# Kernel tuning notes

Hardware: AMD Instinct MI355X
Metric: run time of the kernel (lower is better)

The kernel has to match this reference:

```python
import jax, jax.numpy as jnp
from jax import lax
import numpy as np

B, S, D_CTX = 32, 384, 300
H = 600            # hard-coded in the torch module (torch.zeros([1, 600]))
IN = D_CTX + 3     # context + 3-dim BIO tag embedding


def setup_inputs() -> dict:
    key = jax.random.key(0)
    ks = jax.random.split(key, 12)
    sc = lambda *sh: 1.0 / np.sqrt(sh[-1])
    return {
        "context": jax.random.normal(ks[0], (B, S, D_CTX), jnp.float32),
        "answer_tags": jax.random.randint(ks[1], (B, 1, S), 0, 3),
        "bio_emb": jax.random.normal(ks[2], (3, 3), jnp.float32),
        # GRUCell params (torch layout: W_ih [3H, IN], W_hh [3H, H])
        "W_ih": jax.random.normal(ks[3], (3 * H, IN), jnp.float32) * sc(3 * H, IN),
        "b_ih": jax.random.normal(ks[4], (3 * H,), jnp.float32) * 0.01,
        "W_hh": jax.random.normal(ks[5], (3 * H, H), jnp.float32) * sc(3 * H, H),
        "b_hh": jax.random.normal(ks[6], (3 * H,), jnp.float32) * 0.01,
        "W_lin": jax.random.normal(ks[7], (2 * H, 2 * H), jnp.float32) * sc(2 * H, 2 * H),
        "b_lin": jnp.zeros((2 * H,), jnp.float32),
        "W_g": jax.random.normal(ks[8], (2 * H, 4 * H), jnp.float32) * sc(2 * H, 4 * H),
        "b_g": jnp.zeros((2 * H,), jnp.float32),
        "W_f": jax.random.normal(ks[9], (2 * H, 4 * H), jnp.float32) * sc(2 * H, 4 * H),
        "b_f": jnp.zeros((2 * H,), jnp.float32),
    }


def _gru_scan(xs, W_ih, b_ih, W_hh, b_hh):
    # xs: [T, IN]; hidden carries across ALL steps (the torch code never resets
    # the hidden state between batch elements -- faithful quirk).
    gi_all = xs @ W_ih.T + b_ih            # [T, 3H] precomputed input projections

    def step(h, gi):
        gh = h @ W_hh.T + b_hh             # [3H]
        ir, iz, inn = jnp.split(gi, 3)
        hr, hz, hn = jnp.split(gh, 3)
        r = jax.nn.sigmoid(ir + hr)
        z = jax.nn.sigmoid(iz + hz)
        n = jnp.tanh(inn + r * hn)
        h_new = (1.0 - z) * n + z * h
        return h_new, h_new

    h0 = jnp.zeros((H,), xs.dtype)
    h_last, hs = lax.scan(step, h0, gi_all)
    return h_last, hs                      # [H], [T, H]


def reference(context, answer_tags, bio_emb, W_ih, b_ih, W_hh, b_hh,
              W_lin, b_lin, W_g, b_g, W_f, b_f):
    b, s, _ = context.shape
    tags = bio_emb[answer_tags[:, 0, :]]                    # [B, S, 3]
    emb = jnp.concatenate([tags, context], axis=-1)          # [B, S, IN]

    # Forward direction: one continuous scan over all B*S steps (hidden not reset).
    h_f, fwd = _gru_scan(emb.reshape(b * s, -1), W_ih, b_ih, W_hh, b_hh)
    forward_states = fwd.reshape(b, s, H)

    # Backward direction: words reversed within each batch element; the torch
    # code stores backward_states[b, w] = state after processing word S-1-w.
    h_b, bwd = _gru_scan(emb[:, ::-1, :].reshape(b * s, -1), W_ih, b_ih, W_hh, b_hh)
    backward_states = bwd.reshape(b, s, H)

    all_h = jnp.concatenate([forward_states, backward_states], axis=-1)  # [B,S,2H]

    # calc_attention: the inner state_idx loop OVERWRITES attn[b,:,:] each
    # iteration, so only the LAST state (index S-1) survives, broadcast over S.
    hs = all_h[:, -1, :]                                     # [B, 2H]
    q = hs @ W_lin.T + b_lin                                 # [B, 2H]
    scores = jax.nn.softmax(jnp.einsum('bd,bsd->bs', q, all_h), axis=-1)
    ctx = jnp.einsum('bs,bsd->bd', scores, all_h)            # [B, 2H]
    cat = jnp.concatenate([ctx, hs], axis=-1)                # [B, 4H]
    g = jax.nn.sigmoid(cat @ W_g.T + b_g)
    f = jnp.tanh(cat @ W_f.T + b_f)
    gated = g * f + (1.0 - g) * hs                           # [B, 2H]
    attn = jnp.broadcast_to(gated[:, None, :], (b, s, 2 * H))

    final = jnp.concatenate([h_f, h_b])[None, :]             # [1, 2H]
    return final, attn
```

## Files before the change

kernel.cpp:

```cpp
#include <hip/hip_runtime.h>
#include <math.h>

#define TT    12288
#define HH    600
#define GG    1800
#define INP   303
#define INP_P 304
#define BB    32
#define SS    384
#define D2    1200
#define D4    2400

#define NWG  75
#define JPW  8
#define WROW 608

#define SENT   0xAAAAAAAAu
#define SENT64 0xAAAAAAAAAAAAAAAAull

#define EMB_OFF    0ull
#define WP_OFF     3735552ull
#define GI_OFF     4282752ull
#define HS_OFF     26403808ull
#define Q_OFF      26442208ull
#define CTX_OFF    26480608ull
#define GATED_OFF  26519008ull
#define P_OFF      0ull

__global__ void build_emb(const float* __restrict__ ctx, const int* __restrict__ tags,
                          const float* __restrict__ bio, float* __restrict__ emb) {
    int idx = blockIdx.x * 256 + threadIdx.x;
    if (idx >= TT * INP_P) return;
    int row = idx / INP_P;
    int c = idx - row * INP_P;
    float v;
    if (c < 3)        v = bio[tags[row] * 3 + c];
    else if (c < INP) v = ctx[(size_t)row * 300 + (c - 3)];
    else              v = 0.f;
    emb[idx] = v;
}

__global__ void pad_wih(const float* __restrict__ W, float* __restrict__ Wp) {
    int idx = blockIdx.x * 256 + threadIdx.x;
    if (idx >= GG * INP_P) return;
    int r = idx / INP_P, c = idx - r * INP_P;
    Wp[idx] = (c < INP) ? W[(size_t)r * INP + c] : 0.f;
}

__global__ __launch_bounds__(256) void gemm_gi(const float* __restrict__ A,
                                               const float* __restrict__ Bw,
                                               const float* __restrict__ bias,
                                               float* __restrict__ C) {
    __shared__ float As[16][68];
    __shared__ float Bs[16][68];
    const int tid = threadIdx.x;
    const int bm = blockIdx.x, bn = blockIdx.y;
    const int tx = tid & 15, ty = tid >> 4;
    const int lm = tid >> 2;
    const int lk = (tid & 3) * 4;
    const int gbase = bn * 64;
    float acc[4][4] = {};
    for (int k0 = 0; k0 < INP_P; k0 += 16) {
        float4 av = *(const float4*)(A + (size_t)(bm * 64 + lm) * INP_P + k0 + lk);
        int grow = gbase + lm;
        float4 bv = make_float4(0.f, 0.f, 0.f, 0.f);
        if (grow < GG) bv = *(const float4*)(Bw + (size_t)grow * INP_P + k0 + lk);
        As[lk + 0][lm] = av.x; As[lk + 1][lm] = av.y; As[lk + 2][lm] = av.z; As[lk + 3][lm] = av.w;
        Bs[lk + 0][lm] = bv.x; Bs[lk + 1][lm] = bv.y; Bs[lk + 2][lm] = bv.z; Bs[lk + 3][lm] = bv.w;
        __syncthreads();
#pragma unroll
        for (int kk = 0; kk < 16; ++kk) {
            float4 a4 = *(const float4*)&As[kk][tx * 4];
            float4 b4 = *(const float4*)&Bs[kk][ty * 4];
            acc[0][0] += a4.x * b4.x; acc[0][1] += a4.x * b4.y; acc[0][2] += a4.x * b4.z; acc[0][3] += a4.x * b4.w;
            acc[1][0] += a4.y * b4.x; acc[1][1] += a4.y * b4.y; acc[1][2] += a4.y * b4.z; acc[1][3] += a4.y * b4.w;
            acc[2][0] += a4.z * b4.x; acc[2][1] += a4.z * b4.y; acc[2][2] += a4.z * b4.z; acc[2][3] += a4.z * b4.w;
            acc[3][0] += a4.w * b4.x; acc[3][1] += a4.w * b4.y; acc[3][2] += a4.w * b4.z; acc[3][3] += a4.w * b4.w;
        }
        __syncthreads();
    }
    int g0 = gbase + ty * 4;
    if (g0 < GG) {
        float4 bi4 = *(const float4*)(bias + g0);
#pragma unroll
        for (int i = 0; i < 4; ++i) {
            float4 v = make_float4(acc[i][0] + bi4.x, acc[i][1] + bi4.y,
                                   acc[i][2] + bi4.z, acc[i][3] + bi4.w);
            *(float4*)(C + (size_t)(bm * 64 + tx * 4 + i) * GG + g0) = v;
        }
    }
}

__global__ __launch_bounds__(256) void gru_scan(const float* __restrict__ gi,
                                                const float* __restrict__ Whh,
                                                const float* __restrict__ bhh,
                                                float* __restrict__ out) {
    __shared__ __align__(16) float w_lds[JPW * 3 * WROW];
    __shared__ __align__(16) float h_lds[2][WROW];

    const int tid = threadIdx.x;
    const int chain = blockIdx.x / NWG;
    const int wg = blockIdx.x % NWG;
    const int j0 = wg * JPW;
    const int wave = tid >> 6;
    const int lane = tid & 63;
    const int half = lane >> 5;
    const int s = lane & 31;
    const int j = wave * 2 + half;
    const int jg = j0 + j;

    float* statesOut = out + 1200 + (size_t)chain * TT * 600;
    unsigned long long* statesU64 = (unsigned long long*)statesOut;

    for (int q = tid; q < JPW * 3 * 150; q += 256) {
        int row = q / 150, c4 = (q - row * 150) * 4;
        int jj = row / 3, g = row - jj * 3;
        *(float4*)&w_lds[row * WROW + c4] =
            *(const float4*)(Whh + (size_t)(g * 600 + j0 + jj) * 600 + c4);
    }
    float b_r = 0.f, b_z = 0.f, b_n = 0.f;
    if (s == 0) { b_r = bhh[jg]; b_z = bhh[600 + jg]; b_n = bhh[1200 + jg]; }
    for (int i = tid; i < 2 * WROW; i += 256) h_lds[0][i] = 0.f;
    __syncthreads();

    float gr_c = 0.f, gz_c = 0.f, gn_c = 0.f;
    int si = 0, bi = 0;
    if (s == 0) {
        int r0 = (chain == 0) ? 0 : (SS - 1);
        const float* gp = gi + (size_t)r0 * GG + jg;
        gr_c = gp[0]; gz_c = gp[600]; gn_c = gp[1200];
    }

    float h_own = 0.f;

    for (int t = 0; t < TT; ++t) {
        const int slot = t & 1;
        if (t > 0) {
            if (tid < 150) {
                const unsigned long long* hu = statesU64 + (size_t)(t - 1) * 300 + tid * 2;
                unsigned long long u0, u1;
                for (;;) {
                    u0 = __hip_atomic_load(hu + 0, __ATOMIC_RELAXED, __HIP_MEMORY_SCOPE_AGENT);
                    u1 = __hip_atomic_load(hu + 1, __ATOMIC_RELAXED, __HIP_MEMORY_SCOPE_AGENT);
                    if (u0 != SENT64 && u1 != SENT64) break;
                    __builtin_amdgcn_s_sleep(1);
                }
                float4 hv;
                ((unsigned long long*)&hv)[0] = u0;
                ((unsigned long long*)&hv)[1] = u1;
                *(float4*)&h_lds[slot][tid * 4] = hv;
            }
            __syncthreads();
        }
        float gr_n = gr_c, gz_n = gz_c, gn_n = gn_c;
        int si2 = si + 1, bi2 = bi;
        if (si2 == SS) { si2 = 0; ++bi2; }
        if (s == 0 && t + 1 < TT) {
            int rn = (chain == 0) ? (t + 1) : (bi2 * SS + (SS - 1) - si2);
            const float* gp = gi + (size_t)rn * GG + jg;
            gr_n = gp[0]; gz_n = gp[600]; gn_n = gp[1200];
        }
        float a0 = 0.f, a1 = 0.f, a2 = 0.f;
        if (s < 30) {
            const float* w0 = &w_lds[(j * 3 + 0) * WROW + s * 20];
            const float* w1 = &w_lds[(j * 3 + 1) * WROW + s * 20];
            const float* w2 = &w_lds[(j * 3 + 2) * WROW + s * 20];
            const float* hp = &h_lds[slot][s * 20];
#pragma unroll
            for (int u = 0; u < 5; ++u) {
                float4 hv = *(const float4*)(hp + u * 4);
                float4 x0 = *(const float4*)(w0 + u * 4);
                float4 x1 = *(const float4*)(w1 + u * 4);
                float4 x2 = *(const float4*)(w2 + u * 4);
                a0 += x0.x * hv.x + x0.y * hv.y + x0.z * hv.z + x0.w * hv.w;
                a1 += x1.x * hv.x + x1.y * hv.y + x1.z * hv.z + x1.w * hv.w;
                a2 += x2.x * hv.x + x2.y * hv.y + x2.z * hv.z + x2.w * hv.w;
            }
        }
#pragma unroll
        for (int off = 16; off > 0; off >>= 1) {
            a0 += __shfl_down(a0, off, 32);
            a1 += __shfl_down(a1, off, 32);
            a2 += __shfl_down(a2, off, 32);
        }
        if (s == 0) {
            float r = 1.f / (1.f + __expf(-(gr_c + a0 + b_r)));
            float z = 1.f / (1.f + __expf(-(gz_c + a1 + b_z)));
            float x = gn_c + r * (a2 + b_n);
            float e = __expf(-2.f * fabsf(x));
            float n = copysignf((1.f - e) / (1.f + e), x);
            float hnew = (1.f - z) * n + z * h_own;
            h_own = hnew;
            float partner = __shfl(hnew, (lane + 32) & 63);
            if (half == 0) {
                unsigned long long pk = ((unsigned long long)__float_as_uint(hnew)) |
                                        (((unsigned long long)__float_as_uint(partner)) << 32);
                if (pk == SENT64) pk ^= 1ull;
                __hip_atomic_store(statesU64 + (size_t)t * 300 + (j0 >> 1) + wave, pk,
                                   __ATOMIC_RELAXED, __HIP_MEMORY_SCOPE_AGENT);
            }
            if (t == TT - 1) out[chain * 600 + jg] = hnew;
        }
        gr_c = gr_n; gz_c = gz_n; gn_c = gn_n;
        si = si2; bi = bi2;
    }
}

__global__ __launch_bounds__(256) void attn_qs(const float* __restrict__ Wlin,
                                               const float* __restrict__ blin,
                                               const float* __restrict__ outp,
                                               float* __restrict__ ws) {
    __shared__ float hs_lds[1200];
    const int bi = blockIdx.x, ob = blockIdx.y * 60, tid = threadIdx.x;
    const float* fwdS = outp + 1200;
    const float* bwdS = outp + 1200 + (size_t)TT * 600;
    size_t row = (size_t)(bi * SS + SS - 1) * 600;
    for (int k = tid; k < 600; k += 256) {
        hs_lds[k] = fwdS[row + k];
        hs_lds[600 + k] = bwdS[row + k];
    }
    __syncthreads();
    if (blockIdx.y == 0) {
        float* ws_hs = ws + HS_OFF;
        for (int k = tid; k < 1200; k += 256) ws_hs[bi * 1200 + k] = hs_lds[k];
    }
    float* ws_q = ws + Q_OFF;
    const int wave = tid >> 6, lane = tid & 63;
    for (int i = 0; i < 15; ++i) {
        int o = ob + wave * 15 + i;
        const float* wr = Wlin + (size_t)o * 1200;
        float acc = 0.f;
        for (int k = lane; k < 1200; k += 64) acc += hs_lds[k] * wr[k];
        for (int off = 32; off > 0; off >>= 1) acc += __shfl_down(acc, off);
        if (lane == 0) ws_q[bi * 1200 + o] = acc + blin[o];
    }
}

__global__ __launch_bounds__(256) void attn_logits(const float* __restrict__ outp,
                                                   float* __restrict__ ws) {
    __shared__ float q_lds[1200];
    __shared__ float p_lds[SS];
    __shared__ float red[8];
    const int bi = blockIdx.x, tid = threadIdx.x;
    const float* fwdS = outp + 1200;
    const float* bwdS = outp + 1200 + (size_t)TT * 600;
    const float* ws_q = ws + Q_OFF;
    for (int k = tid; k < 1200; k += 256) q_lds[k] = ws_q[bi * 1200 + k];
    __syncthreads();
    const int wave = tid >> 6, lane = tid & 63;
    for (int s = wave; s < SS; s += 4) {
        size_t base = (size_t)(bi * SS + s) * 600;
        float acc = 0.f;
        for (int k = lane; k < 600; k += 64)
            acc += q_lds[k] * fwdS[base + k] + q_lds[600 + k] * bwdS[base + k];
        for (int off = 32; off > 0; off >>= 1) acc += __shfl_down(acc, off);
        if (lane == 0) p_lds[s] = acc;
    }
    __syncthreads();
    float m = -1e30f;
    for (int i = tid; i < SS; i += 256) m = fmaxf(m, p_lds[i]);
    for (int off = 32; off > 0; off >>= 1) m = fmaxf(m, __shfl_down(m, off));
    if (lane == 0) red[wave] = m;
    __syncthreads();
    m = fmaxf(fmaxf(red[0], red[1]), fmaxf(red[2], red[3]));
    float ssum = 0.f;
    for (int i = tid; i < SS; i += 256) ssum += expf(p_lds[i] - m);
    for (int off = 32; off > 0; off >>= 1) ssum += __shfl_down(ssum, off);
    __syncthreads();
    if (lane == 0) red[wave] = ssum;
    __syncthreads();
    ssum = red[0] + red[1] + red[2] + red[3];
    float inv = 1.f / ssum;
    float* ws_p = ws + P_OFF;
    for (int i = tid; i < SS; i += 256) ws_p[bi * SS + i] = expf(p_lds[i] - m) * inv;
}

__global__ __launch_bounds__(256) void attn_ctxv(const float* __restrict__ outp,
                                                 float* __restrict__ ws) {
    __shared__ float p_lds[SS];
    const int bi = blockIdx.x, d0 = blockIdx.y * 240, tid = threadIdx.x;
    const float* ws_p = ws + P_OFF;
    for (int k = tid; k < SS; k += 256) p_lds[k] = ws_p[bi * SS + k];
    __syncthreads();
    if (tid >= 240) return;
    const int d = d0 + tid;
    const float* fwdS = outp + 1200;
    const float* bwdS = outp + 1200 + (size_t)TT * 600;
    const float* Sb = (d < 600) ? (fwdS + d) : (bwdS + d - 600);
    size_t rbase = (size_t)bi * SS * 600;
    float a0 = 0.f, a1 = 0.f, a2 = 0.f, a3 = 0.f;
#pragma unroll 4
    for (int s = 0; s < SS; s += 4) {
        a0 += p_lds[s + 0] * Sb[rbase + (size_t)(s + 0) * 600];
        a1 += p_lds[s + 1] * Sb[rbase + (size_t)(s + 1) * 600];
        a2 += p_lds[s + 2] * Sb[rbase + (size_t)(s + 2) * 600];
        a3 += p_lds[s + 3] * Sb[rbase + (size_t)(s + 3) * 600];
    }
    (ws + CTX_OFF)[bi * 1200 + d] = (a0 + a1) + (a2 + a3);
}

__global__ __launch_bounds__(256) void attn_gate(const float* __restrict__ Wg,
                                                 const float* __restrict__ bg,
                                                 const float* __restrict__ Wf,
                                                 const float* __restrict__ bf,
                                                 float* __restrict__ ws) {
    __shared__ float cat_lds[2400];
    const int bi = blockIdx.x, ob = blockIdx.y * 60, tid = threadIdx.x;
    const float* ws_ctx = ws + CTX_OFF;
    const float* ws_hs = ws + HS_OFF;
    for (int k = tid; k < 1200; k += 256) {
        cat_lds[k] = ws_ctx[bi * 1200 + k];
        cat_lds[1200 + k] = ws_hs[bi * 1200 + k];
    }
    __syncthreads();
    float* ws_g = ws + GATED_OFF;
    const int wave = tid >> 6, lane = tid & 63;
    for (int i = 0; i < 15; ++i) {
        int o = ob + wave * 15 + i;
        const float* wg = Wg + (size_t)o * D4;
        const float* wf = Wf + (size_t)o * D4;
        float ag = 0.f, af = 0.f;
        for (int k = lane; k < D4; k += 64) {
            float c = cat_lds[k];
            ag += c * wg[k];
            af += c * wf[k];
        }
        for (int off = 32; off > 0; off >>= 1) {
            ag += __shfl_down(ag, off);
            af += __shfl_down(af, off);
        }
        if (lane == 0) {
            float g = 1.f / (1.f + expf(-(ag + bg[o])));
            float f = tanhf(af + bf[o]);
            ws_g[bi * 1200 + o] = g * f + (1.f - g) * cat_lds[1200 + o];
        }
    }
}

__global__ void bcast_attn(const float* __restrict__ ws, float* __restrict__ outp) {
    int idx = blockIdx.x * 256 + threadIdx.x;
    const float4* g4 = (const float4*)(ws + GATED_OFF);
    float4* o4 = (float4*)outp;
    int row = idx / 300;
    int d4 = idx - row * 300;
    int bi = row / SS;
    o4[300 + idx] = g4[bi * 300 + d4];
}

extern "C" void kernel_launch(void* const* d_in, const int* in_sizes, int n_in,
                              void* d_out, int out_size, void* d_ws, size_t ws_size,
                              hipStream_t stream) {
    const float* ctx   = (const float*)d_in[0];
    const int*   tags  = (const int*)d_in[1];
    const float* bio   = (const float*)d_in[2];
    const float* W_ih  = (const float*)d_in[3];
    const float* b_ih  = (const float*)d_in[4];
    const float* W_hh  = (const float*)d_in[5];
    const float* b_hh  = (const float*)d_in[6];
    const float* W_lin = (const float*)d_in[7];
    const float* b_lin = (const float*)d_in[8];
    const float* W_g   = (const float*)d_in[9];
    const float* b_g   = (const float*)d_in[10];
    const float* W_f   = (const float*)d_in[11];
    const float* b_f   = (const float*)d_in[12];
    float* out = (float*)d_out;
    float* ws  = (float*)d_ws;

    hipMemsetAsync(out + 1200, 0xAA, (size_t)2 * TT * 600 * sizeof(float), stream);

    build_emb<<<(TT * INP_P + 255) / 256, 256, 0, stream>>>(ctx, tags, bio, ws + EMB_OFF);
    pad_wih<<<(GG * INP_P + 255) / 256, 256, 0, stream>>>(W_ih, ws + WP_OFF);
    gemm_gi<<<dim3(TT / 64, 29), 256, 0, stream>>>(ws + EMB_OFF, ws + WP_OFF, b_ih, ws + GI_OFF);
    gru_scan<<<2 * NWG, 256, 0, stream>>>(ws + GI_OFF, W_hh, b_hh, out);
    attn_qs<<<dim3(BB, 20), 256, 0, stream>>>(W_lin, b_lin, out, ws);
    attn_logits<<<BB, 256, 0, stream>>>(out, ws);
    attn_ctxv<<<dim3(BB, 5), 256, 0, stream>>>(out, ws);
    attn_gate<<<dim3(BB, 20), 256, 0, stream>>>(W_g, b_g, W_f, b_f, ws);
    bcast_attn<<<14400, 256, 0, stream>>>(ws, out);
}
```

Measured before the change: 22.69 ms.

## Replace per-thread sentinel polling with sharded arrival counters in GRU scan

Each workgroup now bumps one of eight sharded global counters per step, and wave 0 polls those counters until all 75 workgroups of its chain have finished the previous step. It then signals the other waves through an LDS flag. The per-element sentinel loads become a single confirming read with no sleep. The aim is to cut the many scattered global polls on the serial 12288-step recurrence, at the cost of an extra atomic add per step and a counter memset.

New measurement: 26.54 ms. +17.0%, slower.

```diff
diff --git a/kernel.cpp b/kernel.cpp
--- a/kernel.cpp
+++ b/kernel.cpp
@@ -25,6 +25,7 @@
 #define Q_OFF      26442208ull
 #define CTX_OFF    26480608ull
 #define GATED_OFF  26519008ull
+#define COUNT_OFF  26557408ull
 #define P_OFF      0ull
 
 __global__ void build_emb(const float* __restrict__ ctx, const int* __restrict__ tags,
@@ -94,9 +95,11 @@
 __global__ __launch_bounds__(256) void gru_scan(const float* __restrict__ gi,
                                                 const float* __restrict__ Whh,
                                                 const float* __restrict__ bhh,
+                                                float* __restrict__ ws,
                                                 float* __restrict__ out) {
     __shared__ __align__(16) float w_lds[JPW * 3 * WROW];
     __shared__ __align__(16) float h_lds[2][WROW];
+    __shared__ unsigned go_lds;
 
     const int tid = threadIdx.x;
     const int chain = blockIdx.x / NWG;
@@ -111,6 +114,8 @@
 
     float* statesOut = out + 1200 + (size_t)chain * TT * 600;
     unsigned long long* statesU64 = (unsigned long long*)statesOut;
+    unsigned* cnt = (unsigned*)(ws + COUNT_OFF) + (size_t)chain * 512;
+    const unsigned cntk = (lane < 3) ? 10u : 9u;
 
     for (int q = tid; q < JPW * 3 * 150; q += 256) {
         int row = q / 150, c4 = (q - row * 150) * 4;
@@ -121,6 +126,7 @@
     float b_r = 0.f, b_z = 0.f, b_n = 0.f;
     if (s == 0) { b_r = bhh[jg]; b_z = bhh[600 + jg]; b_n = bhh[1200 + jg]; }
     for (int i = tid; i < 2 * WROW; i += 256) h_lds[0][i] = 0.f;
+    if (tid == 0) go_lds = 0u;
     __syncthreads();
 
     float gr_c = 0.f, gz_c = 0.f, gn_c = 0.f;
@@ -136,14 +142,30 @@
     for (int t = 0; t < TT; ++t) {
         const int slot = t & 1;
         if (t > 0) {
+            if (wave == 0) {
+                const unsigned tgt = (unsigned)t * cntk;
+                for (;;) {
+                    bool ok = true;
+                    if (lane < 8)
+                        ok = __hip_atomic_load(cnt + lane * 64, __ATOMIC_RELAXED,
+                                               __HIP_MEMORY_SCOPE_AGENT) >= tgt;
+                    if (__ballot(ok) == ~0ull) break;
+                    __builtin_amdgcn_s_sleep(1);
+                }
+                if (lane == 0)
+                    __hip_atomic_store(&go_lds, (unsigned)t, __ATOMIC_RELAXED,
+                                       __HIP_MEMORY_SCOPE_WORKGROUP);
+            } else if (wave <= 2) {
+                while (__hip_atomic_load(&go_lds, __ATOMIC_RELAXED,
+                                         __HIP_MEMORY_SCOPE_WORKGROUP) < (unsigned)t) {}
+            }
             if (tid < 150) {
                 const unsigned long long* hu = statesU64 + (size_t)(t - 1) * 300 + tid * 2;
-                unsigned long long u0, u1;
-                for (;;) {
+                unsigned long long u0 = __hip_atomic_load(hu + 0, __ATOMIC_RELAXED, __HIP_MEMORY_SCOPE_AGENT);
+                unsigned long long u1 = __hip_atomic_load(hu + 1, __ATOMIC_RELAXED, __HIP_MEMORY_SCOPE_AGENT);
+                while (u0 == SENT64 || u1 == SENT64) {
                     u0 = __hip_atomic_load(hu + 0, __ATOMIC_RELAXED, __HIP_MEMORY_SCOPE_AGENT);
                     u1 = __hip_atomic_load(hu + 1, __ATOMIC_RELAXED, __HIP_MEMORY_SCOPE_AGENT);
-                    if (u0 != SENT64 && u1 != SENT64) break;
-                    __builtin_amdgcn_s_sleep(1);
                 }
                 float4 hv;
                 ((unsigned long long*)&hv)[0] = u0;
@@ -201,6 +223,9 @@
             }
             if (t == TT - 1) out[chain * 600 + jg] = hnew;
         }
+        if (tid == 0)
+            __hip_atomic_fetch_add(cnt + (wg & 7) * 64, 1u,
+                                   __ATOMIC_RELAXED, __HIP_MEMORY_SCOPE_AGENT);
         gr_c = gr_n; gz_c = gz_n; gn_c = gn_n;
         si = si2; bi = bi2;
     }
@@ -367,11 +392,12 @@
     float* ws  = (float*)d_ws;
 
     hipMemsetAsync(out + 1200, 0xAA, (size_t)2 * TT * 600 * sizeof(float), stream);
+    hipMemsetAsync(ws + COUNT_OFF, 0, (size_t)2 * 512 * sizeof(unsigned), stream);
 
     build_emb<<<(TT * INP_P + 255) / 256, 256, 0, stream>>>(ctx, tags, bio, ws + EMB_OFF);
     pad_wih<<<(GG * INP_P + 255) / 256, 256, 0, stream>>>(W_ih, ws + WP_OFF);
     gemm_gi<<<dim3(TT / 64, 29), 256, 0, stream>>>(ws + EMB_OFF, ws + WP_OFF, b_ih, ws + GI_OFF);
-    gru_scan<<<2 * NWG, 256, 0, stream>>>(ws + GI_OFF, W_hh, b_hh, out);
+    gru_scan<<<2 * NWG, 256, 0, stream>>>(ws + GI_OFF, W_hh, b_hh, ws, out);
     attn_qs<<<dim3(BB, 20), 256, 0, stream>>>(W_lin, b_lin, out, ws);
     attn_logits<<<BB, 256, 0, stream>>>(out, ws);
     attn_ctxv<<<dim3(BB, 5), 256, 0, stream>>>(out, ws);
```

## Use step-tagged double-buffered exchange for GRU hidden-state handoff instead of sentinels

Applied to the files above, without the earlier changes.

The recurrent scan used to pass each step's hidden state between workgroups by polling the output state array for a sentinel pattern. That required a large memset of the whole output region before every launch. The scan now writes plain stores to the output and publishes each hidden value, tagged with its step number, into a small two-slot exchange buffer in workspace. Readers poll that buffer until the tags match. This removes the memset and keeps the polled data in a tiny, cache-resident region. In exchange, each value takes 8 bytes, each poller issues more atomic loads, and correctness relies on the two-slot reuse never being overrun and on stale workspace tags not matching.

Measured after the change: 22.08 ms. -2.7%, faster.

```diff
diff --git a/kernel.cpp b/kernel.cpp
--- a/kernel.cpp
+++ b/kernel.cpp
@@ -15,9 +15,6 @@
 #define JPW  8
 #define WROW 608
 
-#define SENT   0xAAAAAAAAu
-#define SENT64 0xAAAAAAAAAAAAAAAAull
-
 #define EMB_OFF    0ull
 #define WP_OFF     3735552ull
 #define GI_OFF     4282752ull
@@ -25,7 +22,10 @@
 #define Q_OFF      26442208ull
 #define CTX_OFF    26480608ull
 #define GATED_OFF  26519008ull
+#define EXCH_OFF   26557408ull
 #define P_OFF      0ull
+
+typedef unsigned long long ull;
 
 __global__ void build_emb(const float* __restrict__ ctx, const int* __restrict__ tags,
                           const float* __restrict__ bio, float* __restrict__ emb) {
@@ -94,6 +94,7 @@
 __global__ __launch_bounds__(256) void gru_scan(const float* __restrict__ gi,
                                                 const float* __restrict__ Whh,
                                                 const float* __restrict__ bhh,
+                                                float* __restrict__ ws,
                                                 float* __restrict__ out) {
     __shared__ __align__(16) float w_lds[JPW * 3 * WROW];
     __shared__ __align__(16) float h_lds[2][WROW];
@@ -110,7 +111,7 @@
     const int jg = j0 + j;
 
     float* statesOut = out + 1200 + (size_t)chain * TT * 600;
-    unsigned long long* statesU64 = (unsigned long long*)statesOut;
+    ull* exch = (ull*)(ws + EXCH_OFF) + (size_t)chain * 1200;
 
     for (int q = tid; q < JPW * 3 * 150; q += 256) {
         int row = q / 150, c4 = (q - row * 150) * 4;
@@ -137,17 +138,22 @@
         const int slot = t & 1;
         if (t > 0) {
             if (tid < 150) {
-                const unsigned long long* hu = statesU64 + (size_t)(t - 1) * 300 + tid * 2;
-                unsigned long long u0, u1;
+                const ull* ep = exch + (size_t)((t - 1) & 1) * 600 + tid * 4;
+                const unsigned tg = (unsigned)(t - 1);
+                ull u0, u1, u2, u3;
                 for (;;) {
-                    u0 = __hip_atomic_load(hu + 0, __ATOMIC_RELAXED, __HIP_MEMORY_SCOPE_AGENT);
-                    u1 = __hip_atomic_load(hu + 1, __ATOMIC_RELAXED, __HIP_MEMORY_SCOPE_AGENT);
-                    if (u0 != SENT64 && u1 != SENT64) break;
+                    u0 = __hip_atomic_load(ep + 0, __ATOMIC_RELAXED, __HIP_MEMORY_SCOPE_AGENT);
+                    u1 = __hip_atomic_load(ep + 1, __ATOMIC_RELAXED, __HIP_MEMORY_SCOPE_AGENT);
+                    u2 = __hip_atomic_load(ep + 2, __ATOMIC_RELAXED, __HIP_MEMORY_SCOPE_AGENT);
+                    u3 = __hip_atomic_load(ep + 3, __ATOMIC_RELAXED, __HIP_MEMORY_SCOPE_AGENT);
+                    if ((unsigned)(u0 >> 32) == tg && (unsigned)(u1 >> 32) == tg &&
+                        (unsigned)(u2 >> 32) == tg && (unsigned)(u3 >> 32) == tg) break;
                     __builtin_amdgcn_s_sleep(1);
                 }
-                float4 hv;
-                ((unsigned long long*)&hv)[0] = u0;
-                ((unsigned long long*)&hv)[1] = u1;
+                float4 hv = make_float4(__uint_as_float((unsigned)u0),
+                                        __uint_as_float((unsigned)u1),
+                                        __uint_as_float((unsigned)u2),
+                                        __uint_as_float((unsigned)u3));
                 *(float4*)&h_lds[slot][tid * 4] = hv;
             }
             __syncthreads();
@@ -191,14 +197,10 @@
             float n = copysignf((1.f - e) / (1.f + e), x);
             float hnew = (1.f - z) * n + z * h_own;
             h_own = hnew;
-            float partner = __shfl(hnew, (lane + 32) & 63);
-            if (half == 0) {
-                unsigned long long pk = ((unsigned long long)__float_as_uint(hnew)) |
-                                        (((unsigned long long)__float_as_uint(partner)) << 32);
-                if (pk == SENT64) pk ^= 1ull;
-                __hip_atomic_store(statesU64 + (size_t)t * 300 + (j0 >> 1) + wave, pk,
-                                   __ATOMIC_RELAXED, __HIP_MEMORY_SCOPE_AGENT);
-            }
+            statesOut[(size_t)t * 600 + jg] = hnew;
+            __hip_atomic_store(exch + (size_t)slot * 600 + jg,
+                               ((ull)(unsigned)t << 32) | (ull)__float_as_uint(hnew),
+                               __ATOMIC_RELAXED, __HIP_MEMORY_SCOPE_AGENT);
             if (t == TT - 1) out[chain * 600 + jg] = hnew;
         }
         gr_c = gr_n; gz_c = gz_n; gn_c = gn_n;
@@ -366,12 +368,10 @@
     float* out = (float*)d_out;
     float* ws  = (float*)d_ws;
 
-    hipMemsetAsync(out + 1200, 0xAA, (size_t)2 * TT * 600 * sizeof(float), stream);
-
     build_emb<<<(TT * INP_P + 255) / 256, 256, 0, stream>>>(ctx, tags, bio, ws + EMB_OFF);
     pad_wih<<<(GG * INP_P + 255) / 256, 256, 0, stream>>>(W_ih, ws + WP_OFF);
     gemm_gi<<<dim3(TT / 64, 29), 256, 0, stream>>>(ws + EMB_OFF, ws + WP_OFF, b_ih, ws + GI_OFF);
-    gru_scan<<<2 * NWG, 256, 0, stream>>>(ws + GI_OFF, W_hh, b_hh, out);
+    gru_scan<<<2 * NWG, 256, 0, stream>>>(ws + GI_OFF, W_hh, b_hh, ws, out);
     attn_qs<<<dim3(BB, 20), 256, 0, stream>>>(W_lin, b_lin, out, ws);
     attn_logits<<<BB, 256, 0, stream>>>(out, ws);
     attn_ctxv<<<dim3(BB, 5), 256, 0, stream>>>(out, ws);
```
